# Kernel optimization log

Hardware: AMD Instinct MI355X
Metric: run time of the kernel (lower is better)

The kernel has to match this reference:

```python
import jax, jax.numpy as jnp
import numpy as np

NUM_HEADS = 16
ROPE_THETA = 10000.0


def _rope(x, cos, sin):
    # x: [B, H, S, d_k]; cos/sin: [S, d_k//2]
    x2 = x.reshape(x.shape[:-1] + (x.shape[-1] // 2, 2))
    x0, x1 = x2[..., 0], x2[..., 1]
    out0 = cos * x0 - sin * x1
    out1 = sin * x0 + cos * x1
    return jnp.stack([out0, out1], axis=-1).reshape(x.shape)


def setup_inputs() -> dict:
    key = jax.random.key(0)
    ks = jax.random.split(key, 5)
    B, S, D = 4, 2048, 1024
    std = float(np.sqrt(2.0 / (D * D)))
    return {
        "x": jax.random.normal(ks[0], (B, S, D), dtype=jnp.float32),
        "WQ": jax.random.normal(ks[1], (D, D), dtype=jnp.float32) * std,
        "WK": jax.random.normal(ks[2], (D, D), dtype=jnp.float32) * std,
        "WV": jax.random.normal(ks[3], (D, D), dtype=jnp.float32) * std,
        "WO": jax.random.normal(ks[4], (D, D), dtype=jnp.float32) * std,
    }


def reference(x, WQ, WK, WV, WO):
    B, S, D = x.shape
    H = NUM_HEADS
    dk = D // H

    def split_heads(t):  # [B, S, D] -> [B, H, S, dk]
        return t.reshape(B, S, H, dk).transpose(0, 2, 1, 3)

    # Projections: stored weights are [out, in], applied as x @ W.T
    Q = split_heads(x @ WQ.T)
    K = split_heads(x @ WK.T)
    V = split_heads(x @ WV.T)

    # RoPE (interleaved pairs, rotation matrix formulation)
    pos = jnp.arange(S, dtype=jnp.float32)[:, None]               # [S, 1]
    dims = jnp.arange(dk // 2, dtype=jnp.float32)[None, :]        # [1, dk/2]
    thetas = pos / (ROPE_THETA ** (2.0 * dims / dk))              # [S, dk/2]
    cos, sin = jnp.cos(thetas), jnp.sin(thetas)
    Q = _rope(Q, cos, sin)
    K = _rope(K, cos, sin)

    # Causal scaled dot-product attention (full score matrix, per original)
    scores = jnp.einsum('bhqd,bhkd->bhqk', Q, K) / jnp.sqrt(jnp.float32(dk))
    mask = jnp.tril(jnp.ones((S, S), dtype=bool))                 # [S, S]
    scores = jnp.where(mask, scores, -jnp.inf)
    attn = jax.nn.softmax(scores, axis=-1)
    out = jnp.einsum('bhqk,bhkd->bhqd', attn, V)                  # [B, H, S, dk]

    merged = out.transpose(0, 2, 1, 3).reshape(B, S, D)
    return merged @ WO.T
```

## Files before the change

kernel.cpp:

```cpp
#include <hip/hip_runtime.h>
#include <stdint.h>


typedef __attribute__((ext_vector_type(8))) __bf16 bf16x8;
typedef __attribute__((ext_vector_type(4))) float f32x4;

typedef __attribute__((address_space(1))) uint32_t AS1u32;
typedef __attribute__((address_space(3))) uint32_t AS3u32;

__device__ __forceinline__ unsigned short f2bf(float f) {
  uint32_t u = __builtin_bit_cast(uint32_t, f);
  u += 0x7fffu + ((u >> 16) & 1u);
  return (unsigned short)(u >> 16);
}
__device__ __forceinline__ float bf2f(unsigned short h) {
  return __builtin_bit_cast(float, (uint32_t)h << 16);
}
__device__ __forceinline__ void lds_load16(const void* g, void* l) {
  __builtin_amdgcn_global_load_lds((AS1u32*)g, (AS3u32*)l, 16, 0, 0);
}
__device__ __forceinline__ f32x4 mfma16(bf16x8 a, bf16x8 b, f32x4 c) {
  return __builtin_amdgcn_mfma_f32_16x16x32_bf16(a, b, c, 0, 0, 0);
}

__global__ void cast_f32_to_bf16x4(const float4* __restrict__ in,
                                   uint2* __restrict__ out, int n4) {
  int i = blockIdx.x * 256 + threadIdx.x;
  if (i >= n4) return;
  float4 v = in[i];
  uint2 o;
  o.x = (uint32_t)f2bf(v.x) | ((uint32_t)f2bf(v.y) << 16);
  o.y = (uint32_t)f2bf(v.z) | ((uint32_t)f2bf(v.w) << 16);
  out[i] = o;
}

__global__ void rope_table_kernel(float* __restrict__ tab) {
  int i = blockIdx.x * 256 + threadIdx.x;
  int s = i >> 5, p = i & 31;
  double ang = (double)s * pow(10000.0, -(double)p / 32.0);
  tab[2 * i]     = (float)cos(ang);
  tab[2 * i + 1] = (float)sin(ang);
}

__global__ void rope_apply_kernel(unsigned short* __restrict__ buf,
                                  const float2* __restrict__ tab, float scale) {
  int i = blockIdx.x * 256 + threadIdx.x;
  int row = i >> 9;
  int pp  = i & 511;
  float2 cs = tab[(row & 2047) * 32 + (pp & 31)];
  uint32_t v = *(uint32_t*)(buf + 2 * (size_t)i);
  float x0 = bf2f((unsigned short)(v & 0xffffu));
  float x1 = bf2f((unsigned short)(v >> 16));
  float o0 = (cs.x * x0 - cs.y * x1) * scale;
  float o1 = (cs.y * x0 + cs.x * x1) * scale;
  *(uint32_t*)(buf + 2 * (size_t)i) =
      (uint32_t)f2bf(o0) | ((uint32_t)f2bf(o1) << 16);
}

template <int MODE>
__global__ __launch_bounds__(256)
void gemm_bt(const unsigned short* __restrict__ A,
             const unsigned short* __restrict__ B,
             unsigned short* __restrict__ Qo,
             unsigned short* __restrict__ Ko,
             unsigned short* __restrict__ Vt,
             float* __restrict__ CF,
             int M, int N, int K) {
  __shared__ unsigned short As[128 * 64];
  __shared__ unsigned short Bs[128 * 64];
  const int tid = threadIdx.x;
  const int lane = tid & 63, wave = tid >> 6;
  const int l16 = lane & 15, g4 = lane >> 4;
  const int wr = wave >> 1, wc = wave & 1;
  const int row0 = blockIdx.y * 128;
  const int col0 = blockIdx.x * 128;

  const f32x4 fz = {0.f, 0.f, 0.f, 0.f};
  f32x4 acc[4][4];
#pragma unroll
  for (int m = 0; m < 4; ++m)
#pragma unroll
    for (int n = 0; n < 4; ++n) acc[m][n] = fz;

  for (int kt = 0; kt < K; kt += 64) {
    __syncthreads();
#pragma unroll
    for (int i = 0; i < 4; ++i) {
      int flat = i * 2048 + tid * 8;
      int r = flat >> 6, c = flat & 63;
      lds_load16(A + (size_t)(row0 + r) * K + kt + c, &As[flat]);
      lds_load16(B + (size_t)(col0 + r) * K + kt + c, &Bs[flat]);
    }
    __syncthreads();
#pragma unroll
    for (int kk = 0; kk < 2; ++kk) {
      bf16x8 af[4], bfr[4];
#pragma unroll
      for (int m = 0; m < 4; ++m)
        af[m] = *(const bf16x8*)&As[(wr * 64 + m * 16 + l16) * 64 + kk * 32 + g4 * 8];
#pragma unroll
      for (int n = 0; n < 4; ++n)
        bfr[n] = *(const bf16x8*)&Bs[(wc * 64 + n * 16 + l16) * 64 + kk * 32 + g4 * 8];
#pragma unroll
      for (int m = 0; m < 4; ++m)
#pragma unroll
        for (int n = 0; n < 4; ++n)
          acc[m][n] = mfma16(af[m], bfr[n], acc[m][n]);
    }
  }

  const int rbase = row0 + wr * 64 + g4 * 4;
  const int cbase = col0 + wc * 64 + l16;
  if (MODE == 1) {
#pragma unroll
    for (int m = 0; m < 4; ++m)
#pragma unroll
      for (int n = 0; n < 4; ++n)
#pragma unroll
        for (int r = 0; r < 4; ++r)
          CF[(size_t)(rbase + m * 16 + r) * N + cbase + n * 16] = acc[m][n][r];
  } else {
    const int seg = col0 >> 10;
    if (seg < 2) {
      unsigned short* O = seg ? Ko : Qo;
      const int cl = cbase - (seg << 10);
#pragma unroll
      for (int m = 0; m < 4; ++m)
#pragma unroll
        for (int n = 0; n < 4; ++n)
#pragma unroll
          for (int r = 0; r < 4; ++r)
            O[(size_t)(rbase + m * 16 + r) * 1024 + cl + n * 16] = f2bf(acc[m][n][r]);
    } else {
#pragma unroll
      for (int m = 0; m < 4; ++m) {
        const int srow = rbase + m * 16;
        const int b = srow >> 11, s = srow & 2047;
#pragma unroll
        for (int n = 0; n < 4; ++n) {
          const int cg = cbase - 2048 + n * 16;
          const int h = cg >> 6, d = cg & 63;
          ushort4 pk;
          pk.x = f2bf(acc[m][n][0]);
          pk.y = f2bf(acc[m][n][1]);
          pk.z = f2bf(acc[m][n][2]);
          pk.w = f2bf(acc[m][n][3]);
          *(ushort4*)(Vt + ((size_t)(b * 16 + h) * 64 + d) * 2048 + s) = pk;
        }
      }
    }
  }
}

__global__ __launch_bounds__(256)
void attn_kernel(const unsigned short* __restrict__ Qb,
                 const unsigned short* __restrict__ Kb,
                 const unsigned short* __restrict__ Vt,
                 unsigned short* __restrict__ AO) {
  __shared__ unsigned short Ks[2][64 * 64];
  __shared__ unsigned short Vs[2][64 * 64];
  __shared__ unsigned short Ps[4][16 * 64];
  const int tid = threadIdx.x;
  const int lane = tid & 63, wave = tid >> 6;
  const int l16 = lane & 15, g4 = lane >> 4;
  const int qt = 31 - blockIdx.x;
  const int bh = blockIdx.y;
  const int b = bh >> 4, h = bh & 15;
  const int q0 = qt << 6;

  const unsigned short* qp =
      Qb + (size_t)(b * 2048 + q0 + wave * 16 + l16) * 1024 + h * 64 + g4 * 8;
  const bf16x8 qf0 = *(const bf16x8*)qp;
  const bf16x8 qf1 = *(const bf16x8*)(qp + 32);

  const unsigned short* kptr[2];
  const unsigned short* vptr[2];
#pragma unroll
  for (int i = 0; i < 2; ++i) {
    int L = i * 256 + tid;
    int r = L >> 3, ch = L & 7;
    int sc8 = ((ch ^ (r & 7)) << 3);
    kptr[i] = Kb + ((size_t)b * 2048 + r) * 1024 + h * 64 + sc8;
    vptr[i] = Vt + ((size_t)bh * 64 + r) * 2048 + sc8;
  }

  const f32x4 fz = {0.f, 0.f, 0.f, 0.f};
  f32x4 acc_o[4];
#pragma unroll
  for (int d = 0; d < 4; ++d) acc_o[d] = fz;
  float mrow[4] = {-1e30f, -1e30f, -1e30f, -1e30f};
  float lrow[4] = {0.f, 0.f, 0.f, 0.f};

  const int qrb = q0 + wave * 16 + g4 * 4;
  const int x7 = l16 & 7;
  const int c0 = (g4 ^ x7) << 3;
  const int pr7 = 4 * (g4 & 1);

#pragma unroll
  for (int i = 0; i < 2; ++i) {
    lds_load16(kptr[i], &Ks[0][(i * 256 + tid) * 8]);
    lds_load16(vptr[i], &Vs[0][(i * 256 + tid) * 8]);
  }
  __syncthreads();

  int cur = 0;
  for (int kt = 0; kt <= qt; ++kt) {
    if (kt < qt) {
#pragma unroll
      for (int i = 0; i < 2; ++i) {
        lds_load16(kptr[i] + (size_t)(kt + 1) * 65536, &Ks[cur ^ 1][(i * 256 + tid) * 8]);
        lds_load16(vptr[i] + (size_t)(kt + 1) * 64,    &Vs[cur ^ 1][(i * 256 + tid) * 8]);
      }
    }

    f32x4 sc[4];
    __builtin_amdgcn_s_setprio(1);
#pragma unroll
    for (int n = 0; n < 4; ++n) {
      f32x4 s = fz;
      s = mfma16(qf0, *(const bf16x8*)&Ks[cur][(n * 16 + l16) * 64 + c0], s);
      s = mfma16(qf1, *(const bf16x8*)&Ks[cur][(n * 16 + l16) * 64 + (c0 ^ 32)], s);
      sc[n] = s;
    }
    __builtin_amdgcn_s_setprio(0);

    if (kt == qt) {
#pragma unroll
      for (int n = 0; n < 4; ++n) {
        int kc = kt * 64 + n * 16 + l16;
#pragma unroll
        for (int r = 0; r < 4; ++r)
          if (kc > qrb + r) sc[n][r] = -1e30f;
      }
    }

    float p[4][4];
#pragma unroll
    for (int r = 0; r < 4; ++r) {
      float rm = fmaxf(fmaxf(sc[0][r], sc[1][r]), fmaxf(sc[2][r], sc[3][r]));
      rm = fmaxf(rm, __shfl_xor(rm, 1));
      rm = fmaxf(rm, __shfl_xor(rm, 2));
      rm = fmaxf(rm, __shfl_xor(rm, 4));
      rm = fmaxf(rm, __shfl_xor(rm, 8));
      float mn = fmaxf(mrow[r], rm);
      float so = __builtin_amdgcn_exp2f(mrow[r] - mn);
      float sum = 0.f;
#pragma unroll
      for (int n = 0; n < 4; ++n) {
        float pv = __builtin_amdgcn_exp2f(sc[n][r] - mn);
        p[n][r] = pv;
        sum += pv;
      }
      sum += __shfl_xor(sum, 1);
      sum += __shfl_xor(sum, 2);
      sum += __shfl_xor(sum, 4);
      sum += __shfl_xor(sum, 8);
      lrow[r] = lrow[r] * so + sum;
      mrow[r] = mn;
#pragma unroll
      for (int d = 0; d < 4; ++d) acc_o[d][r] *= so;
    }

#pragma unroll
    for (int n = 0; n < 4; ++n) {
      int chunkbase = 2 * n + (l16 >> 3);
#pragma unroll
      for (int r = 0; r < 4; ++r) {
        int ch = chunkbase ^ (r + pr7);
        Ps[wave][(g4 * 4 + r) * 64 + ch * 8 + x7] = f2bf(p[n][r]);
      }
    }
    bf16x8 pf0 = *(const bf16x8*)&Ps[wave][l16 * 64 + c0];
    bf16x8 pf1 = *(const bf16x8*)&Ps[wave][l16 * 64 + (c0 ^ 32)];

    __builtin_amdgcn_s_setprio(1);
#pragma unroll
    for (int d = 0; d < 4; ++d) {
      acc_o[d] = mfma16(pf0, *(const bf16x8*)&Vs[cur][(d * 16 + l16) * 64 + c0], acc_o[d]);
      acc_o[d] = mfma16(pf1, *(const bf16x8*)&Vs[cur][(d * 16 + l16) * 64 + (c0 ^ 32)], acc_o[d]);
    }
    __builtin_amdgcn_s_setprio(0);

    __syncthreads();
    cur ^= 1;
  }

  const size_t ob = (size_t)(b * 2048 + q0 + wave * 16 + g4 * 4) * 1024 + h * 64 + l16;
#pragma unroll
  for (int r = 0; r < 4; ++r) {
    float inv = 1.f / lrow[r];
#pragma unroll
    for (int d = 0; d < 4; ++d)
      AO[ob + (size_t)r * 1024 + d * 16] = f2bf(acc_o[d][r] * inv);
  }
}

extern "C" void kernel_launch(void* const* d_in, const int* in_sizes, int n_in,
                              void* d_out, int out_size, void* d_ws, size_t ws_size,
                              hipStream_t stream) {
  const float* x  = (const float*)d_in[0];
  const float* WQ = (const float*)d_in[1];
  const float* WK = (const float*)d_in[2];
  const float* WV = (const float*)d_in[3];
  const float* WO = (const float*)d_in[4];
  float* out = (float*)d_out;

  unsigned short* xb   = (unsigned short*)d_ws;
  unsigned short* wqkv = xb + (size_t)8192 * 1024;
  unsigned short* wo   = wqkv + (size_t)3072 * 1024;
  unsigned short* Qb   = wo + (size_t)1024 * 1024;
  unsigned short* Kb   = Qb + (size_t)8192 * 1024;
  unsigned short* Vt   = Kb + (size_t)8192 * 1024;
  float* tab = (float*)(Vt + (size_t)8192 * 1024);

  cast_f32_to_bf16x4<<<8192, 256, 0, stream>>>((const float4*)x, (uint2*)xb, 8192 * 1024 / 4);
  cast_f32_to_bf16x4<<<1024, 256, 0, stream>>>((const float4*)WQ, (uint2*)wqkv, 1024 * 1024 / 4);
  cast_f32_to_bf16x4<<<1024, 256, 0, stream>>>((const float4*)WK, (uint2*)(wqkv + (size_t)1024 * 1024), 1024 * 1024 / 4);
  cast_f32_to_bf16x4<<<1024, 256, 0, stream>>>((const float4*)WV, (uint2*)(wqkv + (size_t)2048 * 1024), 1024 * 1024 / 4);
  cast_f32_to_bf16x4<<<1024, 256, 0, stream>>>((const float4*)WO, (uint2*)wo, 1024 * 1024 / 4);
  rope_table_kernel<<<256, 256, 0, stream>>>(tab);

  gemm_bt<0><<<dim3(24, 64), 256, 0, stream>>>(xb, wqkv, Qb, Kb, Vt, nullptr, 8192, 3072, 1024);

  rope_apply_kernel<<<16384, 256, 0, stream>>>(Qb, (const float2*)tab, 0.18033688011112042f);
  rope_apply_kernel<<<16384, 256, 0, stream>>>(Kb, (const float2*)tab, 1.0f);

  attn_kernel<<<dim3(32, 64), 256, 0, stream>>>(Qb, Kb, Vt, xb);

  gemm_bt<1><<<dim3(8, 64), 256, 0, stream>>>(xb, wo, nullptr, nullptr, nullptr, out, 8192, 1024, 1024);
}
```

Baseline: 436.0 us.

## Pair complementary causal query tiles per attention block to balance and reuse K/V

```diff
diff --git a/kernel.cpp b/kernel.cpp
--- a/kernel.cpp
+++ b/kernel.cpp
@@ -152,6 +152,82 @@
   }
 }
 
+__device__ __forceinline__ void attn_step(
+    const unsigned short* Ksb, const unsigned short* Vsb, unsigned short* Psw,
+    const bf16x8& q0, const bf16x8& q1, float* mrow, float* lrow,
+    f32x4* acc, int qrbase, bool diag, int kt,
+    int l16, int g4, int c0, int x7, int pr7) {
+  const f32x4 fz = {0.f, 0.f, 0.f, 0.f};
+
+  f32x4 sc[4];
+  __builtin_amdgcn_s_setprio(1);
+#pragma unroll
+  for (int n = 0; n < 4; ++n) {
+    f32x4 s = fz;
+    s = mfma16(q0, *(const bf16x8*)&Ksb[(n * 16 + l16) * 64 + c0], s);
+    s = mfma16(q1, *(const bf16x8*)&Ksb[(n * 16 + l16) * 64 + (c0 ^ 32)], s);
+    sc[n] = s;
+  }
+  __builtin_amdgcn_s_setprio(0);
+
+  if (diag) {
+#pragma unroll
+    for (int n = 0; n < 4; ++n) {
+      int kc = kt * 64 + n * 16 + l16;
+#pragma unroll
+      for (int r = 0; r < 4; ++r)
+        if (kc > qrbase + r) sc[n][r] = -1e30f;
+    }
+  }
+
+  float p[4][4];
+#pragma unroll
+  for (int r = 0; r < 4; ++r) {
+    float rm = fmaxf(fmaxf(sc[0][r], sc[1][r]), fmaxf(sc[2][r], sc[3][r]));
+    rm = fmaxf(rm, __shfl_xor(rm, 1));
+    rm = fmaxf(rm, __shfl_xor(rm, 2));
+    rm = fmaxf(rm, __shfl_xor(rm, 4));
+    rm = fmaxf(rm, __shfl_xor(rm, 8));
+    float mn = fmaxf(mrow[r], rm);
+    float so = __builtin_amdgcn_exp2f(mrow[r] - mn);
+    float sum = 0.f;
+#pragma unroll
+    for (int n = 0; n < 4; ++n) {
+      float pv = __builtin_amdgcn_exp2f(sc[n][r] - mn);
+      p[n][r] = pv;
+      sum += pv;
+    }
+    sum += __shfl_xor(sum, 1);
+    sum += __shfl_xor(sum, 2);
+    sum += __shfl_xor(sum, 4);
+    sum += __shfl_xor(sum, 8);
+    lrow[r] = lrow[r] * so + sum;
+    mrow[r] = mn;
+#pragma unroll
+    for (int d = 0; d < 4; ++d) acc[d][r] *= so;
+  }
+
+#pragma unroll
+  for (int n = 0; n < 4; ++n) {
+    int chunkbase = 2 * n + (l16 >> 3);
+#pragma unroll
+    for (int r = 0; r < 4; ++r) {
+      int ch = chunkbase ^ (r + pr7);
+      Psw[(g4 * 4 + r) * 64 + ch * 8 + x7] = f2bf(p[n][r]);
+    }
+  }
+  bf16x8 pf0 = *(const bf16x8*)&Psw[l16 * 64 + c0];
+  bf16x8 pf1 = *(const bf16x8*)&Psw[l16 * 64 + (c0 ^ 32)];
+
+  __builtin_amdgcn_s_setprio(1);
+#pragma unroll
+  for (int d = 0; d < 4; ++d) {
+    acc[d] = mfma16(pf0, *(const bf16x8*)&Vsb[(d * 16 + l16) * 64 + c0], acc[d]);
+    acc[d] = mfma16(pf1, *(const bf16x8*)&Vsb[(d * 16 + l16) * 64 + (c0 ^ 32)], acc[d]);
+  }
+  __builtin_amdgcn_s_setprio(0);
+}
+
 __global__ __launch_bounds__(256)
 void attn_kernel(const unsigned short* __restrict__ Qb,
                  const unsigned short* __restrict__ Kb,
@@ -163,15 +239,16 @@
   const int tid = threadIdx.x;
   const int lane = tid & 63, wave = tid >> 6;
   const int l16 = lane & 15, g4 = lane >> 4;
-  const int qt = 31 - blockIdx.x;
+  const int qa = blockIdx.x, qb = 31 - qa;
   const int bh = blockIdx.y;
   const int b = bh >> 4, h = bh & 15;
-  const int q0 = qt << 6;
-
-  const unsigned short* qp =
-      Qb + (size_t)(b * 2048 + q0 + wave * 16 + l16) * 1024 + h * 64 + g4 * 8;
-  const bf16x8 qf0 = *(const bf16x8*)qp;
-  const bf16x8 qf1 = *(const bf16x8*)(qp + 32);
+
+  const unsigned short* qpa =
+      Qb + (size_t)(b * 2048 + qa * 64 + wave * 16 + l16) * 1024 + h * 64 + g4 * 8;
+  const unsigned short* qpb =
+      Qb + (size_t)(b * 2048 + qb * 64 + wave * 16 + l16) * 1024 + h * 64 + g4 * 8;
+  const bf16x8 qfa0 = *(const bf16x8*)qpa, qfa1 = *(const bf16x8*)(qpa + 32);
+  const bf16x8 qfb0 = *(const bf16x8*)qpb, qfb1 = *(const bf16x8*)(qpb + 32);
 
   const unsigned short* kptr[2];
   const unsigned short* vptr[2];
@@ -185,13 +262,17 @@
   }
 
   const f32x4 fz = {0.f, 0.f, 0.f, 0.f};
-  f32x4 acc_o[4];
-#pragma unroll
-  for (int d = 0; d < 4; ++d) acc_o[d] = fz;
-  float mrow[4] = {-1e30f, -1e30f, -1e30f, -1e30f};
-  float lrow[4] = {0.f, 0.f, 0.f, 0.f};
-
-  const int qrb = q0 + wave * 16 + g4 * 4;
+  f32x4 acc_a[4], acc_b[4];
+#pragma unroll
+  for (int d = 0; d < 4; ++d) { acc_a[d] = fz; acc_b[d] = fz; }
+  float ma[4], la[4], mb[4], lb[4];
+#pragma unroll
+  for (int r = 0; r < 4; ++r) {
+    ma[r] = -1e30f; mb[r] = -1e30f; la[r] = 0.f; lb[r] = 0.f;
+  }
+
+  const int qra  = qa * 64 + wave * 16 + g4 * 4;
+  const int qrb_ = qb * 64 + wave * 16 + g4 * 4;
   const int x7 = l16 & 7;
   const int c0 = (g4 ^ x7) << 3;
   const int pr7 = 4 * (g4 & 1);
@@ -204,94 +285,42 @@
   __syncthreads();
 
   int cur = 0;
-  for (int kt = 0; kt <= qt; ++kt) {
-    if (kt < qt) {
+  for (int kt = 0; kt <= qb; ++kt) {
+    if (kt < qb) {
 #pragma unroll
       for (int i = 0; i < 2; ++i) {
         lds_load16(kptr[i] + (size_t)(kt + 1) * 65536, &Ks[cur ^ 1][(i * 256 + tid) * 8]);
         lds_load16(vptr[i] + (size_t)(kt + 1) * 64,    &Vs[cur ^ 1][(i * 256 + tid) * 8]);
       }
     }
-
-    f32x4 sc[4];
-    __builtin_amdgcn_s_setprio(1);
-#pragma unroll
-    for (int n = 0; n < 4; ++n) {
-      f32x4 s = fz;
-      s = mfma16(qf0, *(const bf16x8*)&Ks[cur][(n * 16 + l16) * 64 + c0], s);
-      s = mfma16(qf1, *(const bf16x8*)&Ks[cur][(n * 16 + l16) * 64 + (c0 ^ 32)], s);
-      sc[n] = s;
-    }
-    __builtin_amdgcn_s_setprio(0);
-
-    if (kt == qt) {
-#pragma unroll
-      for (int n = 0; n < 4; ++n) {
-        int kc = kt * 64 + n * 16 + l16;
-#pragma unroll
-        for (int r = 0; r < 4; ++r)
-          if (kc > qrb + r) sc[n][r] = -1e30f;
-      }
-    }
-
-    float p[4][4];
-#pragma unroll
-    for (int r = 0; r < 4; ++r) {
-      float rm = fmaxf(fmaxf(sc[0][r], sc[1][r]), fmaxf(sc[2][r], sc[3][r]));
-      rm = fmaxf(rm, __shfl_xor(rm, 1));
-      rm = fmaxf(rm, __shfl_xor(rm, 2));
-      rm = fmaxf(rm, __shfl_xor(rm, 4));
-      rm = fmaxf(rm, __shfl_xor(rm, 8));
-      float mn = fmaxf(mrow[r], rm);
-      float so = __builtin_amdgcn_exp2f(mrow[r] - mn);
-      float sum = 0.f;
-#pragma unroll
-      for (int n = 0; n < 4; ++n) {
-        float pv = __builtin_amdgcn_exp2f(sc[n][r] - mn);
-        p[n][r] = pv;
-        sum += pv;
-      }
-      sum += __shfl_xor(sum, 1);
-      sum += __shfl_xor(sum, 2);
-      sum += __shfl_xor(sum, 4);
-      sum += __shfl_xor(sum, 8);
-      lrow[r] = lrow[r] * so + sum;
-      mrow[r] = mn;
-#pragma unroll
-      for (int d = 0; d < 4; ++d) acc_o[d][r] *= so;
-    }
-
-#pragma unroll
-    for (int n = 0; n < 4; ++n) {
-      int chunkbase = 2 * n + (l16 >> 3);
-#pragma unroll
-      for (int r = 0; r < 4; ++r) {
-        int ch = chunkbase ^ (r + pr7);
-        Ps[wave][(g4 * 4 + r) * 64 + ch * 8 + x7] = f2bf(p[n][r]);
-      }
-    }
-    bf16x8 pf0 = *(const bf16x8*)&Ps[wave][l16 * 64 + c0];
-    bf16x8 pf1 = *(const bf16x8*)&Ps[wave][l16 * 64 + (c0 ^ 32)];
-
-    __builtin_amdgcn_s_setprio(1);
-#pragma unroll
-    for (int d = 0; d < 4; ++d) {
-      acc_o[d] = mfma16(pf0, *(const bf16x8*)&Vs[cur][(d * 16 + l16) * 64 + c0], acc_o[d]);
-      acc_o[d] = mfma16(pf1, *(const bf16x8*)&Vs[cur][(d * 16 + l16) * 64 + (c0 ^ 32)], acc_o[d]);
-    }
-    __builtin_amdgcn_s_setprio(0);
-
+    attn_step(Ks[cur], Vs[cur], Ps[wave], qfb0, qfb1, mb, lb, acc_b, qrb_,
+              kt == qb, kt, l16, g4, c0, x7, pr7);
+    if (kt <= qa)
+      attn_step(Ks[cur], Vs[cur], Ps[wave], qfa0, qfa1, ma, la, acc_a, qra,
+                kt == qa, kt, l16, g4, c0, x7, pr7);
     __syncthreads();
     cur ^= 1;
   }
 
-  const size_t ob = (size_t)(b * 2048 + q0 + wave * 16 + g4 * 4) * 1024 + h * 64 + l16;
-#pragma unroll
-  for (int r = 0; r < 4; ++r) {
-    float inv = 1.f / lrow[r];
-#pragma unroll
-    for (int d = 0; d < 4; ++d)
-      AO[ob + (size_t)r * 1024 + d * 16] = f2bf(acc_o[d][r] * inv);
+  {
+    const size_t ob = (size_t)(b * 2048 + qb * 64 + wave * 16 + g4 * 4) * 1024 + h * 64 + l16;
+#pragma unroll
+    for (int r = 0; r < 4; ++r) {
+      float inv = 1.f / lb[r];
+#pragma unroll
+      for (int d = 0; d < 4; ++d)
+        AO[ob + (size_t)r * 1024 + d * 16] = f2bf(acc_b[d][r] * inv);
+    }
+  }
+  {
+    const size_t ob = (size_t)(b * 2048 + qa * 64 + wave * 16 + g4 * 4) * 1024 + h * 64 + l16;
+#pragma unroll
+    for (int r = 0; r < 4; ++r) {
+      float inv = 1.f / la[r];
+#pragma unroll
+      for (int d = 0; d < 4; ++d)
+        AO[ob + (size_t)r * 1024 + d * 16] = f2bf(acc_a[d][r] * inv);
+    }
   }
 }
 
@@ -325,7 +354,7 @@
   rope_apply_kernel<<<16384, 256, 0, stream>>>(Qb, (const float2*)tab, 0.18033688011112042f);
   rope_apply_kernel<<<16384, 256, 0, stream>>>(Kb, (const float2*)tab, 1.0f);
 
-  attn_kernel<<<dim3(32, 64), 256, 0, stream>>>(Qb, Kb, Vt, xb);
+  attn_kernel<<<dim3(16, 64), 256, 0, stream>>>(Qb, Kb, Vt, xb);
 
   gemm_bt<1><<<dim3(8, 64), 256, 0, stream>>>(xb, wo, nullptr, nullptr, nullptr, out, 8192, 1024, 1024);
 }
```

Result: faster. 364.7 us (-16.4%).
